# Optimization experiments

Hardware: AMD Instinct MI355X
Metric: run time of the kernel (lower is better)

Reference implementation:

```python
import jax, jax.numpy as jnp
import numpy as np
import math

NEG = -1000000.0

def setup_inputs() -> dict:
    key = jax.random.key(0)
    k1, k2, k3, k4 = jax.random.split(key, 4)
    B, S, D = 64, 1024, 64
    query = jax.random.normal(k1, (B, S, D), dtype=jnp.float32)
    key_t = jax.random.normal(k2, (B, S, D), dtype=jnp.float32)
    value = jax.random.normal(k3, (B, S, D), dtype=jnp.float32)
    valid_lens = jax.random.randint(k4, (B,), 1, S + 1, dtype=jnp.int32)
    return {"query": query, "key": key_t, "value": value, "valid_lens": valid_lens}

def reference(query, key, value, valid_lens):
    # query/key/value: [B, S, D]; valid_lens: [B]
    d = query.shape[-1]
    scores = jnp.einsum('bqd,bkd->bqk', query, key) / math.sqrt(d)
    Sk = key.shape[1]
    # 1D valid_lens -> same mask for every query row (repeat_interleave semantics)
    mask = jnp.arange(Sk)[None, None, :] < valid_lens[:, None, None]  # [B,1,Sk]
    scores = jnp.where(mask, scores, NEG)
    weights = jax.nn.softmax(scores, axis=-1)
    # dropout p=0.0 -> identity
    return jnp.einsum('bqk,bkd->bqd', weights, value)
```

## Files before the change

### kernel.cpp

```cpp
#include <hip/hip_runtime.h>
#include <hip/hip_bf16.h>
#include <cstdint>


typedef __attribute__((ext_vector_type(8))) short short8;
typedef __attribute__((ext_vector_type(4))) float f32x4;

#define B_   64
#define S_   1024
#define D_   64
#define BQ   64
#define BK   64
#define KPAD 72

__device__ __forceinline__ uint32_t pk2(float a, float b) {
    float2 t; t.x = a; t.y = b;
    union { __hip_bfloat162 h; uint32_t u; } c;
    c.h = __float22bfloat162_rn(t);
    return c.u;
}

__global__ __launch_bounds__(256, 4)
void attn_fwd(const float* __restrict__ Q, const float* __restrict__ K,
              const float* __restrict__ V, const int* __restrict__ VL,
              float* __restrict__ Out) {
    __shared__ __align__(16) unsigned short lK [BK * KPAD];
    __shared__ __align__(16) unsigned short lVt[D_ * 64];
    __shared__ __align__(16) unsigned short lP [4 * 16 * KPAD];

    const int tid  = threadIdx.x;
    const int wave = tid >> 6;
    const int lane = tid & 63;
    const int col  = lane & 15;
    const int quad = lane >> 4;

    const int bid  = blockIdx.x;
    const int b    = (bid & 7) * 8 + (bid >> 7);
    const int q0   = ((bid >> 3) & 15) * BQ;
    const int vlen = VL[b];
    const int ntiles = (vlen + BK - 1) / BK;

    const int T  = tid >> 4;
    const int m  = tid & 15;
    const int Tl = T & 3;
    const int cb = T >> 2;
    const int dcs = m >> 1;
    const int sws = ((dcs & 1) << 2) | (dcs >> 1);

    const float* Kb = K + (size_t)b * S_ * D_ + 4 * m;
    const float* Vb = V + (size_t)b * S_ * D_ + 4 * m;

    float4 kr[4], vr[4];
    #pragma unroll
    for (int j = 0; j < 4; ++j) {
        const int row = 2 * T + (j >> 1) * 32 + (j & 1);
        kr[j] = *(const float4*)(Kb + (size_t)row * D_);
        vr[j] = *(const float4*)(Vb + (size_t)row * D_);
    }

    short8 qa[2];
    {
        const int qrow = q0 + wave * 16 + col;
        const float* qp = Q + ((size_t)b * S_ + qrow) * D_ + quad * 8;
        #pragma unroll
        for (int c = 0; c < 2; ++c) {
            float4 x0 = *(const float4*)(qp + c * 32);
            float4 x1 = *(const float4*)(qp + c * 32 + 4);
            union { uint32_t u[4]; short8 s; } qq;
            qq.u[0] = pk2(x0.x, x0.y);
            qq.u[1] = pk2(x0.z, x0.w);
            qq.u[2] = pk2(x1.x, x1.y);
            qq.u[3] = pk2(x1.z, x1.w);
            qa[c] = qq.s;
        }
    }

    f32x4 ofrag[4];
    #pragma unroll
    for (int dt = 0; dt < 4; ++dt) ofrag[dt] = (f32x4){0.f, 0.f, 0.f, 0.f};
    float lsum = 0.f;

    const float cexp = 0.18033688011112042f;
    unsigned short* pw = &lP[wave * 16 * KPAD];

    for (int kt = 0; kt < ntiles; ++kt) {
        const int kbase = kt * BK;

        __syncthreads();

        #pragma unroll
        for (int j = 0; j < 4; ++j) {
            const int row = 2 * T + (j >> 1) * 32 + (j & 1);
            uint2 kv;
            kv.x = pk2(kr[j].x, kr[j].y);
            kv.y = pk2(kr[j].z, kr[j].w);
            *(uint2*)&lK[row * KPAD + 4 * m] = kv;
        }
        #pragma unroll
        for (int i = 0; i < 2; ++i) {
            const int p = (cb + 4 * i) ^ sws;
            unsigned short* base = &lVt[p * 8 + 2 * Tl];
            const float4 va = vr[2 * i], vb2 = vr[2 * i + 1];
            *(uint32_t*)&base[(4 * m + 0) * 64] = pk2(va.x, vb2.x);
            *(uint32_t*)&base[(4 * m + 1) * 64] = pk2(va.y, vb2.y);
            *(uint32_t*)&base[(4 * m + 2) * 64] = pk2(va.z, vb2.z);
            *(uint32_t*)&base[(4 * m + 3) * 64] = pk2(va.w, vb2.w);
        }

        __syncthreads();

        if (kt + 1 < ntiles) {
            const size_t off = (size_t)(kt + 1) * BK * D_;
            #pragma unroll
            for (int j = 0; j < 4; ++j) {
                const int row = 2 * T + (j >> 1) * 32 + (j & 1);
                kr[j] = *(const float4*)(Kb + off + (size_t)row * D_);
                vr[j] = *(const float4*)(Vb + off + (size_t)row * D_);
            }
        }

        f32x4 sfrag[4];
        #pragma unroll
        for (int ct = 0; ct < 4; ++ct) {
            f32x4 acc = (f32x4){0.f, 0.f, 0.f, 0.f};
            #pragma unroll
            for (int c = 0; c < 2; ++c) {
                short8 kf = *(const short8*)&lK[(ct * 16 + col) * KPAD + c * 32 + quad * 8];
                acc = __builtin_amdgcn_mfma_f32_16x16x32_bf16(kf, qa[c], acc, 0, 0, 0);
            }
            sfrag[ct] = acc;
        }

        if (kbase + BK <= vlen) {
            #pragma unroll
            for (int ct = 0; ct < 4; ++ct) {
                float e0 = __builtin_amdgcn_exp2f(sfrag[ct][0] * cexp);
                float e1 = __builtin_amdgcn_exp2f(sfrag[ct][1] * cexp);
                float e2 = __builtin_amdgcn_exp2f(sfrag[ct][2] * cexp);
                float e3 = __builtin_amdgcn_exp2f(sfrag[ct][3] * cexp);
                lsum += (e0 + e1) + (e2 + e3);
                uint2 pk; pk.x = pk2(e0, e1); pk.y = pk2(e2, e3);
                *(uint2*)&pw[col * KPAD + ct * 16 + quad * 4] = pk;
            }
        } else {
            #pragma unroll
            for (int ct = 0; ct < 4; ++ct) {
                const int kv0 = kbase + ct * 16 + quad * 4;
                float e[4];
                #pragma unroll
                for (int rr = 0; rr < 4; ++rr) {
                    e[rr] = (kv0 + rr < vlen)
                          ? __builtin_amdgcn_exp2f(sfrag[ct][rr] * cexp) : 0.0f;
                    lsum += e[rr];
                }
                uint2 pk; pk.x = pk2(e[0], e[1]); pk.y = pk2(e[2], e[3]);
                *(uint2*)&pw[col * KPAD + ct * 16 + quad * 4] = pk;
            }
        }

        #pragma unroll
        for (int kc = 0; kc < 2; ++kc) {
            short8 pa = *(const short8*)&pw[col * KPAD + kc * 32 + quad * 8];
            #pragma unroll
            for (int dt = 0; dt < 4; ++dt) {
                const int sr = ((col >> 3) << 2) | dt;
                const int p  = (kc * 4 + quad) ^ sr;
                short8 vb = *(const short8*)&lVt[(dt * 16 + col) * 64 + p * 8];
                ofrag[dt] = __builtin_amdgcn_mfma_f32_16x16x32_bf16(pa, vb, ofrag[dt], 0, 0, 0);
            }
        }
    }

    float s = lsum;
    s += __shfl_xor(s, 16, 64);
    s += __shfl_xor(s, 32, 64);
    const int qrow0 = q0 + wave * 16 + quad * 4;
    #pragma unroll
    for (int rr = 0; rr < 4; ++rr) {
        const float inv = 1.0f / __shfl(s, quad * 4 + rr, 64);
        float* op = Out + ((size_t)b * S_ + qrow0 + rr) * D_ + col;
        #pragma unroll
        for (int dt = 0; dt < 4; ++dt)
            op[dt * 16] = ofrag[dt][rr] * inv;
    }
}

extern "C" void kernel_launch(void* const* d_in, const int* in_sizes, int n_in,
                              void* d_out, int out_size, void* d_ws, size_t ws_size,
                              hipStream_t stream) {
    const float* Q  = (const float*)d_in[0];
    const float* K  = (const float*)d_in[1];
    const float* V  = (const float*)d_in[2];
    const int*   VL = (const int*)d_in[3];
    float* Out = (float*)d_out;
    dim3 grid(B_ * (S_ / BQ));
    attn_fwd<<<grid, 256, 0, stream>>>(Q, K, V, VL, Out);
}
```

Before: 115.8 us.

## Double-buffer K/V in LDS and pass P through cross-lane shuffles

K and V tiles now live in two LDS buffers. The next tile is staged into the alternate buffer after the PV MFMAs, so each iteration needs one barrier instead of two. The per-wave P scratch buffer in LDS is removed, and the exponentiated scores are rearranged into the MFMA A-operand layout with wave shuffles and selects. This cuts LDS traffic and barrier count, at the cost of more LDS for the K/V buffers and extra shuffle and select instructions.

```diff
diff --git a/kernel.cpp b/kernel.cpp
--- a/kernel.cpp
+++ b/kernel.cpp
@@ -20,13 +20,36 @@
     return c.u;
 }
 
+__device__ __forceinline__ void stage_kv(unsigned short* __restrict__ lk,
+                                         unsigned short* __restrict__ lvt,
+                                         const float4* kr, const float4* vr,
+                                         int T, int m, int Tl, int cb, int sws) {
+    #pragma unroll
+    for (int j = 0; j < 4; ++j) {
+        const int row = 2 * T + (j >> 1) * 32 + (j & 1);
+        uint2 kv;
+        kv.x = pk2(kr[j].x, kr[j].y);
+        kv.y = pk2(kr[j].z, kr[j].w);
+        *(uint2*)&lk[row * KPAD + 4 * m] = kv;
+    }
+    #pragma unroll
+    for (int i = 0; i < 2; ++i) {
+        const int p = (cb + 4 * i) ^ sws;
+        unsigned short* base = &lvt[p * 8 + 2 * Tl];
+        const float4 va = vr[2 * i], vb2 = vr[2 * i + 1];
+        *(uint32_t*)&base[(4 * m + 0) * 64] = pk2(va.x, vb2.x);
+        *(uint32_t*)&base[(4 * m + 1) * 64] = pk2(va.y, vb2.y);
+        *(uint32_t*)&base[(4 * m + 2) * 64] = pk2(va.z, vb2.z);
+        *(uint32_t*)&base[(4 * m + 3) * 64] = pk2(va.w, vb2.w);
+    }
+}
+
 __global__ __launch_bounds__(256, 4)
 void attn_fwd(const float* __restrict__ Q, const float* __restrict__ K,
               const float* __restrict__ V, const int* __restrict__ VL,
               float* __restrict__ Out) {
-    __shared__ __align__(16) unsigned short lK [BK * KPAD];
-    __shared__ __align__(16) unsigned short lVt[D_ * 64];
-    __shared__ __align__(16) unsigned short lP [4 * 16 * KPAD];
+    __shared__ __align__(16) unsigned short lK [2][BK * KPAD];
+    __shared__ __align__(16) unsigned short lVt[2][D_ * 64];
 
     const int tid  = threadIdx.x;
     const int wave = tid >> 6;
@@ -81,31 +104,12 @@
     float lsum = 0.f;
 
     const float cexp = 0.18033688011112042f;
-    unsigned short* pw = &lP[wave * 16 * KPAD];
+
+    stage_kv(&lK[0][0], &lVt[0][0], kr, vr, T, m, Tl, cb, sws);
 
     for (int kt = 0; kt < ntiles; ++kt) {
         const int kbase = kt * BK;
-
-        __syncthreads();
-
-        #pragma unroll
-        for (int j = 0; j < 4; ++j) {
-            const int row = 2 * T + (j >> 1) * 32 + (j & 1);
-            uint2 kv;
-            kv.x = pk2(kr[j].x, kr[j].y);
-            kv.y = pk2(kr[j].z, kr[j].w);
-            *(uint2*)&lK[row * KPAD + 4 * m] = kv;
-        }
-        #pragma unroll
-        for (int i = 0; i < 2; ++i) {
-            const int p = (cb + 4 * i) ^ sws;
-            unsigned short* base = &lVt[p * 8 + 2 * Tl];
-            const float4 va = vr[2 * i], vb2 = vr[2 * i + 1];
-            *(uint32_t*)&base[(4 * m + 0) * 64] = pk2(va.x, vb2.x);
-            *(uint32_t*)&base[(4 * m + 1) * 64] = pk2(va.y, vb2.y);
-            *(uint32_t*)&base[(4 * m + 2) * 64] = pk2(va.z, vb2.z);
-            *(uint32_t*)&base[(4 * m + 3) * 64] = pk2(va.w, vb2.w);
-        }
+        const int cur   = kt & 1;
 
         __syncthreads();
 
@@ -125,12 +129,13 @@
             f32x4 acc = (f32x4){0.f, 0.f, 0.f, 0.f};
             #pragma unroll
             for (int c = 0; c < 2; ++c) {
-                short8 kf = *(const short8*)&lK[(ct * 16 + col) * KPAD + c * 32 + quad * 8];
+                short8 kf = *(const short8*)&lK[cur][(ct * 16 + col) * KPAD + c * 32 + quad * 8];
                 acc = __builtin_amdgcn_mfma_f32_16x16x32_bf16(kf, qa[c], acc, 0, 0, 0);
             }
             sfrag[ct] = acc;
         }
 
+        uint32_t u[4][2];
         if (kbase + BK <= vlen) {
             #pragma unroll
             for (int ct = 0; ct < 4; ++ct) {
@@ -139,8 +144,8 @@
                 float e2 = __builtin_amdgcn_exp2f(sfrag[ct][2] * cexp);
                 float e3 = __builtin_amdgcn_exp2f(sfrag[ct][3] * cexp);
                 lsum += (e0 + e1) + (e2 + e3);
-                uint2 pk; pk.x = pk2(e0, e1); pk.y = pk2(e2, e3);
-                *(uint2*)&pw[col * KPAD + ct * 16 + quad * 4] = pk;
+                u[ct][0] = pk2(e0, e1);
+                u[ct][1] = pk2(e2, e3);
             }
         } else {
             #pragma unroll
@@ -153,22 +158,60 @@
                           ? __builtin_amdgcn_exp2f(sfrag[ct][rr] * cexp) : 0.0f;
                     lsum += e[rr];
                 }
-                uint2 pk; pk.x = pk2(e[0], e[1]); pk.y = pk2(e[2], e[3]);
-                *(uint2*)&pw[col * KPAD + ct * 16 + quad * 4] = pk;
+                u[ct][0] = pk2(e[0], e[1]);
+                u[ct][1] = pk2(e[2], e[3]);
+            }
+        }
+
+        short8 pa[2];
+        {
+            const bool h1  = (quad & 2) != 0;
+            uint32_t A[2][2], Bp[2][2];
+            #pragma unroll
+            for (int w = 0; w < 2; ++w) {
+                A[0][w]  = h1 ? u[1][w] : u[0][w];
+                A[1][w]  = h1 ? u[3][w] : u[2][w];
+                Bp[0][w] = h1 ? u[0][w] : u[1][w];
+                Bp[1][w] = h1 ? u[2][w] : u[3][w];
+            }
+            uint32_t S16[2][2], S32[2][2], S48[2][2];
+            #pragma unroll
+            for (int kc = 0; kc < 2; ++kc)
+                #pragma unroll
+                for (int w = 0; w < 2; ++w) {
+                    S16[kc][w] = (uint32_t)__shfl_xor((int)A[kc][w],  16, 64);
+                    S32[kc][w] = (uint32_t)__shfl_xor((int)Bp[kc][w], 32, 64);
+                    S48[kc][w] = (uint32_t)__shfl_xor((int)Bp[kc][w], 48, 64);
+                }
+            const bool qb0 = (quad & 1) != 0;
+            const bool qb1 = (quad & 2) != 0;
+            #pragma unroll
+            for (int kc = 0; kc < 2; ++kc) {
+                union { uint32_t u4[4]; short8 s; } P;
+                #pragma unroll
+                for (int w = 0; w < 2; ++w) {
+                    P.u4[w]     = qb0 ? (qb1 ? S16[kc][w] : S48[kc][w])
+                                      : (qb1 ? S32[kc][w] : A[kc][w]);
+                    P.u4[2 + w] = qb0 ? (qb1 ? A[kc][w]   : S32[kc][w])
+                                      : (qb1 ? S48[kc][w] : S16[kc][w]);
+                }
+                pa[kc] = P.s;
             }
         }
 
         #pragma unroll
         for (int kc = 0; kc < 2; ++kc) {
-            short8 pa = *(const short8*)&pw[col * KPAD + kc * 32 + quad * 8];
             #pragma unroll
             for (int dt = 0; dt < 4; ++dt) {
                 const int sr = ((col >> 3) << 2) | dt;
                 const int p  = (kc * 4 + quad) ^ sr;
-                short8 vb = *(const short8*)&lVt[(dt * 16 + col) * 64 + p * 8];
-                ofrag[dt] = __builtin_amdgcn_mfma_f32_16x16x32_bf16(pa, vb, ofrag[dt], 0, 0, 0);
-            }
-        }
+                short8 vb = *(const short8*)&lVt[cur][(dt * 16 + col) * 64 + p * 8];
+                ofrag[dt] = __builtin_amdgcn_mfma_f32_16x16x32_bf16(pa[kc], vb, ofrag[dt], 0, 0, 0);
+            }
+        }
+
+        if (kt + 1 < ntiles)
+            stage_kv(&lK[cur ^ 1][0], &lVt[cur ^ 1][0], kr, vr, T, m, Tl, cb, sws);
     }
 
     float s = lsum;
```

Result: slower. 126.4 us (+9.1%).

## Load K/V straight into MFMA registers and split keys across waves

Applied to the files above, without the earlier changes.

Drops the LDS staging of K and transposed V. Each wave now loads its K/V fragments from global memory directly into MFMA operand layout and keeps the softmax probabilities in registers, using the 16x16x16 bf16 MFMA for the PV product. Waves are arranged as 2 query groups by 2 key halves, and the two partial outputs and row sums are combined through LDS at the end. This removes the per-tile barriers and LDS traffic, at the cost of the register prefetch of the next tile, duplicated global K/V reads across waves, and more register pressure.

```diff
diff --git a/kernel.cpp b/kernel.cpp
--- a/kernel.cpp
+++ b/kernel.cpp
@@ -4,6 +4,7 @@
 
 
 typedef __attribute__((ext_vector_type(8))) short short8;
+typedef __attribute__((ext_vector_type(4))) short short4v;
 typedef __attribute__((ext_vector_type(4))) float f32x4;
 
 #define B_   64
@@ -11,7 +12,10 @@
 #define D_   64
 #define BQ   64
 #define BK   64
-#define KPAD 72
+
+__device__ __forceinline__ f32x4 mfma16(short4v a, short4v b, f32x4 c) {
+    return __builtin_amdgcn_mfma_f32_16x16x16bf16_1k(a, b, c, 0, 0, 0);
+}
 
 __device__ __forceinline__ uint32_t pk2(float a, float b) {
     float2 t; t.x = a; t.y = b;
@@ -24,15 +28,16 @@
 void attn_fwd(const float* __restrict__ Q, const float* __restrict__ K,
               const float* __restrict__ V, const int* __restrict__ VL,
               float* __restrict__ Out) {
-    __shared__ __align__(16) unsigned short lK [BK * KPAD];
-    __shared__ __align__(16) unsigned short lVt[D_ * 64];
-    __shared__ __align__(16) unsigned short lP [4 * 16 * KPAD];
+    __shared__ __align__(16) float lO[2 * 32 * 68];
+    __shared__ float lL[2][2][16];
 
     const int tid  = threadIdx.x;
     const int wave = tid >> 6;
     const int lane = tid & 63;
     const int col  = lane & 15;
     const int quad = lane >> 4;
+    const int wq   = wave >> 1;
+    const int wk   = wave & 1;
 
     const int bid  = blockIdx.x;
     const int b    = (bid & 7) * 8 + (bid >> 7);
@@ -40,28 +45,13 @@
     const int vlen = VL[b];
     const int ntiles = (vlen + BK - 1) / BK;
 
-    const int T  = tid >> 4;
-    const int m  = tid & 15;
-    const int Tl = T & 3;
-    const int cb = T >> 2;
-    const int dcs = m >> 1;
-    const int sws = ((dcs & 1) << 2) | (dcs >> 1);
-
-    const float* Kb = K + (size_t)b * S_ * D_ + 4 * m;
-    const float* Vb = V + (size_t)b * S_ * D_ + 4 * m;
-
-    float4 kr[4], vr[4];
+    const float* Kw = K + (size_t)b * S_ * D_ + (size_t)(32 * wk + col) * D_ + quad * 8;
+    const float* Vw = V + (size_t)b * S_ * D_ + (size_t)(32 * wk + quad * 4) * D_ + 4 * col;
+
+    short8 qa[2][2];
     #pragma unroll
-    for (int j = 0; j < 4; ++j) {
-        const int row = 2 * T + (j >> 1) * 32 + (j & 1);
-        kr[j] = *(const float4*)(Kb + (size_t)row * D_);
-        vr[j] = *(const float4*)(Vb + (size_t)row * D_);
-    }
-
-    short8 qa[2];
-    {
-        const int qrow = q0 + wave * 16 + col;
-        const float* qp = Q + ((size_t)b * S_ + qrow) * D_ + quad * 8;
+    for (int qg = 0; qg < 2; ++qg) {
+        const float* qp = Q + ((size_t)b * S_ + q0 + 32 * wq + 16 * qg + col) * D_ + quad * 8;
         #pragma unroll
         for (int c = 0; c < 2; ++c) {
             float4 x0 = *(const float4*)(qp + c * 32);
@@ -71,117 +61,159 @@
             qq.u[1] = pk2(x0.z, x0.w);
             qq.u[2] = pk2(x1.x, x1.y);
             qq.u[3] = pk2(x1.z, x1.w);
-            qa[c] = qq.s;
-        }
-    }
-
-    f32x4 ofrag[4];
+            qa[qg][c] = qq.s;
+        }
+    }
+
+    f32x4 ofrag[2][4];
     #pragma unroll
-    for (int dt = 0; dt < 4; ++dt) ofrag[dt] = (f32x4){0.f, 0.f, 0.f, 0.f};
-    float lsum = 0.f;
+    for (int qg = 0; qg < 2; ++qg)
+        #pragma unroll
+        for (int dt = 0; dt < 4; ++dt) ofrag[qg][dt] = (f32x4){0.f, 0.f, 0.f, 0.f};
+    float lsum[2] = {0.f, 0.f};
 
     const float cexp = 0.18033688011112042f;
-    unsigned short* pw = &lP[wave * 16 * KPAD];
-
+
+    #pragma unroll 1
     for (int kt = 0; kt < ntiles; ++kt) {
         const int kbase = kt * BK;
 
-        __syncthreads();
-
-        #pragma unroll
-        for (int j = 0; j < 4; ++j) {
-            const int row = 2 * T + (j >> 1) * 32 + (j & 1);
-            uint2 kv;
-            kv.x = pk2(kr[j].x, kr[j].y);
-            kv.y = pk2(kr[j].z, kr[j].w);
-            *(uint2*)&lK[row * KPAD + 4 * m] = kv;
-        }
-        #pragma unroll
-        for (int i = 0; i < 2; ++i) {
-            const int p = (cb + 4 * i) ^ sws;
-            unsigned short* base = &lVt[p * 8 + 2 * Tl];
-            const float4 va = vr[2 * i], vb2 = vr[2 * i + 1];
-            *(uint32_t*)&base[(4 * m + 0) * 64] = pk2(va.x, vb2.x);
-            *(uint32_t*)&base[(4 * m + 1) * 64] = pk2(va.y, vb2.y);
-            *(uint32_t*)&base[(4 * m + 2) * 64] = pk2(va.z, vb2.z);
-            *(uint32_t*)&base[(4 * m + 3) * 64] = pk2(va.w, vb2.w);
-        }
-
-        __syncthreads();
-
-        if (kt + 1 < ntiles) {
-            const size_t off = (size_t)(kt + 1) * BK * D_;
-            #pragma unroll
-            for (int j = 0; j < 4; ++j) {
-                const int row = 2 * T + (j >> 1) * 32 + (j & 1);
-                kr[j] = *(const float4*)(Kb + off + (size_t)row * D_);
-                vr[j] = *(const float4*)(Vb + off + (size_t)row * D_);
-            }
-        }
-
-        f32x4 sfrag[4];
-        #pragma unroll
-        for (int ct = 0; ct < 4; ++ct) {
-            f32x4 acc = (f32x4){0.f, 0.f, 0.f, 0.f};
+        float4 kx[2][2][2];
+        #pragma unroll
+        for (int mg = 0; mg < 2; ++mg)
             #pragma unroll
             for (int c = 0; c < 2; ++c) {
-                short8 kf = *(const short8*)&lK[(ct * 16 + col) * KPAD + c * 32 + quad * 8];
-                acc = __builtin_amdgcn_mfma_f32_16x16x32_bf16(kf, qa[c], acc, 0, 0, 0);
-            }
-            sfrag[ct] = acc;
-        }
-
+                const float* p = Kw + (size_t)(kbase + 16 * mg) * D_ + c * 32;
+                kx[mg][c][0] = *(const float4*)(p);
+                kx[mg][c][1] = *(const float4*)(p + 4);
+            }
+        float4 vx[2][4];
+        #pragma unroll
+        for (int mg = 0; mg < 2; ++mg)
+            #pragma unroll
+            for (int j = 0; j < 4; ++j)
+                vx[mg][j] = *(const float4*)(Vw + (size_t)(kbase + 16 * mg + j) * D_);
+
+        short8 kf[2][2];
+        #pragma unroll
+        for (int mg = 0; mg < 2; ++mg)
+            #pragma unroll
+            for (int c = 0; c < 2; ++c) {
+                union { uint32_t u[4]; short8 s; } kk;
+                kk.u[0] = pk2(kx[mg][c][0].x, kx[mg][c][0].y);
+                kk.u[1] = pk2(kx[mg][c][0].z, kx[mg][c][0].w);
+                kk.u[2] = pk2(kx[mg][c][1].x, kx[mg][c][1].y);
+                kk.u[3] = pk2(kx[mg][c][1].z, kx[mg][c][1].w);
+                kf[mg][c] = kk.s;
+            }
+
+        f32x4 sf[2][2];
+        #pragma unroll
+        for (int mg = 0; mg < 2; ++mg)
+            #pragma unroll
+            for (int qg = 0; qg < 2; ++qg) {
+                f32x4 acc = (f32x4){0.f, 0.f, 0.f, 0.f};
+                acc = __builtin_amdgcn_mfma_f32_16x16x32_bf16(kf[mg][0], qa[qg][0], acc, 0, 0, 0);
+                acc = __builtin_amdgcn_mfma_f32_16x16x32_bf16(kf[mg][1], qa[qg][1], acc, 0, 0, 0);
+                sf[mg][qg] = acc;
+            }
+
+        short4v pb[2][2];
         if (kbase + BK <= vlen) {
             #pragma unroll
-            for (int ct = 0; ct < 4; ++ct) {
-                float e0 = __builtin_amdgcn_exp2f(sfrag[ct][0] * cexp);
-                float e1 = __builtin_amdgcn_exp2f(sfrag[ct][1] * cexp);
-                float e2 = __builtin_amdgcn_exp2f(sfrag[ct][2] * cexp);
-                float e3 = __builtin_amdgcn_exp2f(sfrag[ct][3] * cexp);
-                lsum += (e0 + e1) + (e2 + e3);
-                uint2 pk; pk.x = pk2(e0, e1); pk.y = pk2(e2, e3);
-                *(uint2*)&pw[col * KPAD + ct * 16 + quad * 4] = pk;
-            }
+            for (int mg = 0; mg < 2; ++mg)
+                #pragma unroll
+                for (int qg = 0; qg < 2; ++qg) {
+                    float e0 = __builtin_amdgcn_exp2f(sf[mg][qg][0] * cexp);
+                    float e1 = __builtin_amdgcn_exp2f(sf[mg][qg][1] * cexp);
+                    float e2 = __builtin_amdgcn_exp2f(sf[mg][qg][2] * cexp);
+                    float e3 = __builtin_amdgcn_exp2f(sf[mg][qg][3] * cexp);
+                    lsum[qg] += (e0 + e1) + (e2 + e3);
+                    union { uint32_t u[2]; short4v s; } pp;
+                    pp.u[0] = pk2(e0, e1);
+                    pp.u[1] = pk2(e2, e3);
+                    pb[mg][qg] = pp.s;
+                }
         } else {
             #pragma unroll
-            for (int ct = 0; ct < 4; ++ct) {
-                const int kv0 = kbase + ct * 16 + quad * 4;
-                float e[4];
+            for (int mg = 0; mg < 2; ++mg)
                 #pragma unroll
-                for (int rr = 0; rr < 4; ++rr) {
-                    e[rr] = (kv0 + rr < vlen)
-                          ? __builtin_amdgcn_exp2f(sfrag[ct][rr] * cexp) : 0.0f;
-                    lsum += e[rr];
+                for (int qg = 0; qg < 2; ++qg) {
+                    const int kv0 = kbase + 32 * wk + 16 * mg + quad * 4;
+                    float e[4];
+                    #pragma unroll
+                    for (int r = 0; r < 4; ++r) {
+                        e[r] = (kv0 + r < vlen)
+                             ? __builtin_amdgcn_exp2f(sf[mg][qg][r] * cexp) : 0.0f;
+                        lsum[qg] += e[r];
+                    }
+                    union { uint32_t u[2]; short4v s; } pp;
+                    pp.u[0] = pk2(e[0], e[1]);
+                    pp.u[1] = pk2(e[2], e[3]);
+                    pb[mg][qg] = pp.s;
                 }
-                uint2 pk; pk.x = pk2(e[0], e[1]); pk.y = pk2(e[2], e[3]);
-                *(uint2*)&pw[col * KPAD + ct * 16 + quad * 4] = pk;
-            }
-        }
-
-        #pragma unroll
-        for (int kc = 0; kc < 2; ++kc) {
-            short8 pa = *(const short8*)&pw[col * KPAD + kc * 32 + quad * 8];
+        }
+
+        #pragma unroll
+        for (int mg = 0; mg < 2; ++mg) {
+            short4v va[4];
             #pragma unroll
             for (int dt = 0; dt < 4; ++dt) {
-                const int sr = ((col >> 3) << 2) | dt;
-                const int p  = (kc * 4 + quad) ^ sr;
-                short8 vb = *(const short8*)&lVt[(dt * 16 + col) * 64 + p * 8];
-                ofrag[dt] = __builtin_amdgcn_mfma_f32_16x16x32_bf16(pa, vb, ofrag[dt], 0, 0, 0);
-            }
-        }
-    }
-
-    float s = lsum;
-    s += __shfl_xor(s, 16, 64);
-    s += __shfl_xor(s, 32, 64);
-    const int qrow0 = q0 + wave * 16 + quad * 4;
+                union { uint32_t u[2]; short4v s; } vv;
+                vv.u[0] = pk2(vx[mg][0][dt], vx[mg][1][dt]);
+                vv.u[1] = pk2(vx[mg][2][dt], vx[mg][3][dt]);
+                va[dt] = vv.s;
+            }
+            #pragma unroll
+            for (int qg = 0; qg < 2; ++qg)
+                #pragma unroll
+                for (int dt = 0; dt < 4; ++dt)
+                    ofrag[qg][dt] = mfma16(va[dt], pb[mg][qg], ofrag[qg][dt]);
+        }
+    }
+
     #pragma unroll
-    for (int rr = 0; rr < 4; ++rr) {
-        const float inv = 1.0f / __shfl(s, quad * 4 + rr, 64);
-        float* op = Out + ((size_t)b * S_ + qrow0 + rr) * D_ + col;
-        #pragma unroll
-        for (int dt = 0; dt < 4; ++dt)
-            op[dt * 16] = ofrag[dt][rr] * inv;
+    for (int qg = 0; qg < 2; ++qg) {
+        lsum[qg] += __shfl_xor(lsum[qg], 16, 64);
+        lsum[qg] += __shfl_xor(lsum[qg], 32, 64);
+    }
+
+    float* lo = &lO[wq * 32 * 68];
+    if (wk == 1) {
+        #pragma unroll
+        for (int qg = 0; qg < 2; ++qg)
+            #pragma unroll
+            for (int reg = 0; reg < 4; ++reg) {
+                float4 t;
+                t.x = ofrag[qg][0][reg];
+                t.y = ofrag[qg][1][reg];
+                t.z = ofrag[qg][2][reg];
+                t.w = ofrag[qg][3][reg];
+                *(float4*)&lo[(16 * qg + col) * 68 + 16 * quad + 4 * reg] = t;
+            }
+        if (quad == 0) {
+            lL[wq][0][col] = lsum[0];
+            lL[wq][1][col] = lsum[1];
+        }
+    }
+    __syncthreads();
+    if (wk == 0) {
+        #pragma unroll
+        for (int qg = 0; qg < 2; ++qg) {
+            const float linv = 1.0f / (lsum[qg] + lL[wq][qg][col]);
+            float* op = Out + ((size_t)b * S_ + q0 + 32 * wq + 16 * qg + col) * D_
+                        + 16 * quad;
+            #pragma unroll
+            for (int reg = 0; reg < 4; ++reg) {
+                float4 p = *(const float4*)&lo[(16 * qg + col) * 68 + 16 * quad + 4 * reg];
+                float4 o;
+                o.x = (ofrag[qg][0][reg] + p.x) * linv;
+                o.y = (ofrag[qg][1][reg] + p.y) * linv;
+                o.z = (ofrag[qg][2][reg] + p.z) * linv;
+                o.w = (ofrag[qg][3][reg] + p.w) * linv;
+                *(float4*)(op + 4 * reg) = o;
+            }
+        }
     }
 }
 
```

Result: slower. 152.0 us (+31.2%).

## Keep softmax probabilities in registers and feed PV MFMA directly, dropping LDS P

Applied to the files above, without the earlier changes.

Passes the exponentiated scores straight from the QK accumulator registers as the B operand of 16x16x16 bf16 MFMAs, computing O transposed. This removes the per-tile LDS write and read of P and its shared buffer. V is read from the existing swizzled transposed LDS layout in 4-element chunks. The output store becomes vectorized float4 writes with a single per-lane normalizer. In exchange it uses twice as many smaller MFMA instructions and narrower LDS reads of V, which may cause bank conflicts.

```diff
diff --git a/kernel.cpp b/kernel.cpp
--- a/kernel.cpp
+++ b/kernel.cpp
@@ -4,6 +4,7 @@
 
 
 typedef __attribute__((ext_vector_type(8))) short short8;
+typedef __attribute__((ext_vector_type(4))) short short4v;
 typedef __attribute__((ext_vector_type(4))) float f32x4;
 
 #define B_   64
@@ -13,6 +14,10 @@
 #define BK   64
 #define KPAD 72
 
+__device__ __forceinline__ f32x4 mfma16(short4v a, short4v b, f32x4 c) {
+    return __builtin_amdgcn_mfma_f32_16x16x16bf16_1k(a, b, c, 0, 0, 0);
+}
+
 __device__ __forceinline__ uint32_t pk2(float a, float b) {
     float2 t; t.x = a; t.y = b;
     union { __hip_bfloat162 h; uint32_t u; } c;
@@ -26,7 +31,6 @@
               float* __restrict__ Out) {
     __shared__ __align__(16) unsigned short lK [BK * KPAD];
     __shared__ __align__(16) unsigned short lVt[D_ * 64];
-    __shared__ __align__(16) unsigned short lP [4 * 16 * KPAD];
 
     const int tid  = threadIdx.x;
     const int wave = tid >> 6;
@@ -81,7 +85,7 @@
     float lsum = 0.f;
 
     const float cexp = 0.18033688011112042f;
-    unsigned short* pw = &lP[wave * 16 * KPAD];
+    const int sws_v = (((col >> 1) & 1) << 2) | (col >> 2);
 
     for (int kt = 0; kt < ntiles; ++kt) {
         const int kbase = kt * BK;
@@ -131,6 +135,7 @@
             sfrag[ct] = acc;
         }
 
+        short4v pb[4];
         if (kbase + BK <= vlen) {
             #pragma unroll
             for (int ct = 0; ct < 4; ++ct) {
@@ -139,8 +144,10 @@
                 float e2 = __builtin_amdgcn_exp2f(sfrag[ct][2] * cexp);
                 float e3 = __builtin_amdgcn_exp2f(sfrag[ct][3] * cexp);
                 lsum += (e0 + e1) + (e2 + e3);
-                uint2 pk; pk.x = pk2(e0, e1); pk.y = pk2(e2, e3);
-                *(uint2*)&pw[col * KPAD + ct * 16 + quad * 4] = pk;
+                union { uint32_t u[2]; short4v s; } pp;
+                pp.u[0] = pk2(e0, e1);
+                pp.u[1] = pk2(e2, e3);
+                pb[ct] = pp.s;
             }
         } else {
             #pragma unroll
@@ -153,35 +160,39 @@
                           ? __builtin_amdgcn_exp2f(sfrag[ct][rr] * cexp) : 0.0f;
                     lsum += e[rr];
                 }
-                uint2 pk; pk.x = pk2(e[0], e[1]); pk.y = pk2(e[2], e[3]);
-                *(uint2*)&pw[col * KPAD + ct * 16 + quad * 4] = pk;
-            }
-        }
-
-        #pragma unroll
-        for (int kc = 0; kc < 2; ++kc) {
-            short8 pa = *(const short8*)&pw[col * KPAD + kc * 32 + quad * 8];
+                union { uint32_t u[2]; short4v s; } pp;
+                pp.u[0] = pk2(e[0], e[1]);
+                pp.u[1] = pk2(e[2], e[3]);
+                pb[ct] = pp.s;
+            }
+        }
+
+        #pragma unroll
+        for (int ct = 0; ct < 4; ++ct) {
+            const int K0 = ct * 16 + quad * 4;
+            const int p  = (((K0 >> 3) & 3) + 4 * (K0 >> 5)) ^ sws_v;
+            const int o8 = K0 & 7;
             #pragma unroll
             for (int dt = 0; dt < 4; ++dt) {
-                const int sr = ((col >> 3) << 2) | dt;
-                const int p  = (kc * 4 + quad) ^ sr;
-                short8 vb = *(const short8*)&lVt[(dt * 16 + col) * 64 + p * 8];
-                ofrag[dt] = __builtin_amdgcn_mfma_f32_16x16x32_bf16(pa, vb, ofrag[dt], 0, 0, 0);
-            }
-        }
-    }
-
-    float s = lsum;
-    s += __shfl_xor(s, 16, 64);
-    s += __shfl_xor(s, 32, 64);
-    const int qrow0 = q0 + wave * 16 + quad * 4;
+                short4v va = *(const short4v*)&lVt[(4 * col + dt) * 64 + p * 8 + o8];
+                ofrag[dt] = mfma16(va, pb[ct], ofrag[dt]);
+            }
+        }
+    }
+
+    float sred = lsum;
+    sred += __shfl_xor(sred, 16, 64);
+    sred += __shfl_xor(sred, 32, 64);
+    const float inv = 1.0f / sred;
+    float* op = Out + ((size_t)b * S_ + q0 + wave * 16 + col) * D_ + 16 * quad;
     #pragma unroll
-    for (int rr = 0; rr < 4; ++rr) {
-        const float inv = 1.0f / __shfl(s, quad * 4 + rr, 64);
-        float* op = Out + ((size_t)b * S_ + qrow0 + rr) * D_ + col;
-        #pragma unroll
-        for (int dt = 0; dt < 4; ++dt)
-            op[dt * 16] = ofrag[dt][rr] * inv;
+    for (int reg = 0; reg < 4; ++reg) {
+        float4 o;
+        o.x = ofrag[0][reg] * inv;
+        o.y = ofrag[1][reg] * inv;
+        o.z = ofrag[2][reg] * inv;
+        o.w = ofrag[3][reg] * inv;
+        *(float4*)(op + 4 * reg) = o;
     }
 }
 
```

Result: no change. 117.8 us (+1.7%).
